# Performance work log

Measured on AMD Instinct MI355X. Metric: run time of the kernel, lower is better.

## Reference

```python
import jax, jax.numpy as jnp
import numpy as np

N = 50000
E = 800000
IN_DIM = 128
HID = 128
OUT = 40


def setup_inputs() -> dict:
    key = jax.random.key(0)
    k1, k2, k3, k4, k5 = jax.random.split(key, 5)
    x = jax.random.normal(k1, (N, IN_DIM), dtype=jnp.float32)
    edge_index = jax.random.randint(k2, (2, E), 0, N, dtype=jnp.int64)
    # Glorot-ish init for GCNConv weights, zero bias (PyG default bias=True)
    W1 = jax.random.normal(k3, (IN_DIM, HID), dtype=jnp.float32) / np.sqrt(IN_DIM)
    b1 = jnp.zeros((HID,), dtype=jnp.float32)
    W2 = jax.random.normal(k4, (HID, OUT), dtype=jnp.float32) / np.sqrt(HID)
    b2 = jnp.zeros((OUT,), dtype=jnp.float32)
    return {"x": x, "edge_index": edge_index, "W1": W1, "b1": b1, "W2": W2, "b2": b2}


def _gcn_norm(edge_index, n_nodes):
    """Add self-loops and compute symmetric GCN normalization per edge.
    Returns (src, dst, norm) with len E + n_nodes."""
    loops = jnp.arange(n_nodes, dtype=edge_index.dtype)
    src = jnp.concatenate([edge_index[0], loops])
    dst = jnpp_concat = jnp.concatenate([edge_index[1], loops])
    dst = jnp.concatenate([edge_index[1], loops])
    deg = jax.ops.segment_sum(jnp.ones_like(dst, dtype=jnp.float32), dst,
                              num_segments=n_nodes)
    dinv = jnp.where(deg > 0, jax.lax.rsqrt(deg), 0.0)
    norm = dinv[src] * dinv[dst]  # [E + N]
    return src, dst, norm


def _gcn_conv(x, src, dst, norm, W, b, n_nodes):
    xw = x @ W                                  # [N, F_out] transform first
    msg = xw[src] * norm[:, None]               # gather + scale, [E+N, F_out]
    out = jax.ops.segment_sum(msg, dst, num_segments=n_nodes)  # scatter-add
    return out + b


def reference(x, edge_index, W1, b1, W2, b2):
    n = x.shape[0]
    src, dst, norm = _gcn_norm(edge_index, n)
    h = _gcn_conv(x, src, dst, norm, W1, b1, n)
    h = jax.nn.relu(h)
    # dropout is identity in eval mode (training=False)
    h = _gcn_conv(h, src, dst, norm, W2, b2, n)
    return jax.nn.softmax(h, axis=1)
```

## Files before the change

kernel.cpp:

```cpp
#include <hip/hip_runtime.h>
#include <hip/hip_fp16.h>

#define IN_DIM 128
#define HID    128
#define OUTC   40
#define CAP    64
#define LSTR   136

typedef _Float16 f16x8 __attribute__((ext_vector_type(8)));
typedef _Float16 f16x4 __attribute__((ext_vector_type(4)));
typedef float    f32x4 __attribute__((ext_vector_type(4)));

__global__ __launch_bounds__(256) void k_scatter(const int* __restrict__ edge, int* __restrict__ cnt,
                                                 int* __restrict__ col,
                                                 const float* __restrict__ W1, const float* __restrict__ W2,
                                                 _Float16* __restrict__ W1T, _Float16* __restrict__ W2T,
                                                 int E, int n, int nbE) {
  int b = blockIdx.x;
  if (b < nbE) {
    int e = b * 256 + threadIdx.x;
    if (e >= E) return;
    int sv = edge[e];
    int d  = edge[E + e];
    if ((unsigned)d >= (unsigned)n || (unsigned)sv >= (unsigned)n) return;
    int pos = atomicAdd(&cnt[d], 1);
    if (pos < CAP) col[(size_t)d * CAP + pos] = sv;
  } else {
    int t = (b - nbE) * 256 + threadIdx.x;
    if (t < 128 * 128) {
      int nn = t >> 7, kk = t & 127;
      W1T[t] = (_Float16)W1[kk * 128 + nn];
    }
    if (t < 48 * 128) {
      int nn = t >> 7, kk = t & 127;
      W2T[t] = (nn < OUTC) ? (_Float16)W2[kk * OUTC + nn] : (_Float16)0.f;
    }
  }
}


__global__ __launch_bounds__(256) void k_gemm1(const float* __restrict__ x, const _Float16* __restrict__ W1T,
                                               const int* __restrict__ cnt, __half* __restrict__ out, int n) {
  __shared__ _Float16 sW[128 * LSTR];
  __shared__ _Float16 sX[64 * LSTR];
  int tid = threadIdx.x;
  int i0  = blockIdx.x * 64;

  {
    const uint4* src = (const uint4*)W1T;
    for (int idx = tid; idx < 2048; idx += 256) {
      int nn = idx >> 4, c = idx & 15;
      *(uint4*)&sW[nn * LSTR + c * 8] = src[nn * 16 + c];
    }
  }
  for (int idx = tid; idx < 2048; idx += 256) {
    int r = idx >> 5, c = idx & 31;
    int row = i0 + r;
    float4 v = (row < n) ? *(const float4*)&x[(size_t)row * IN_DIM + c * 4]
                         : make_float4(0.f, 0.f, 0.f, 0.f);
    f16x4 hv; hv[0] = (_Float16)v.x; hv[1] = (_Float16)v.y; hv[2] = (_Float16)v.z; hv[3] = (_Float16)v.w;
    *(f16x4*)&sX[r * LSTR + c * 4] = hv;
  }
  __syncthreads();

  int wv = tid >> 6, lane = tid & 63;
  int m = lane & 15, quad = lane >> 4;

  const _Float16* ax = &sX[(16 * wv + m) * LSTR + quad * 8];
  f16x8 a0 = *(const f16x8*)(ax);
  f16x8 a1 = *(const f16x8*)(ax + 32);
  f16x8 a2 = *(const f16x8*)(ax + 64);
  f16x8 a3 = *(const f16x8*)(ax + 96);

  int base_row = i0 + 16 * wv + quad * 4;
  float dvr[4];
#pragma unroll
  for (int r = 0; r < 4; ++r) {
    int row = base_row + r;
    dvr[r] = (row < n) ? rsqrtf((float)(cnt[row] + 1)) : 0.f;
  }

#pragma unroll
  for (int t = 0; t < 8; ++t) {
    const _Float16* bx = &sW[(t * 16 + m) * LSTR + quad * 8];
    f16x8 b0 = *(const f16x8*)(bx);
    f16x8 b1 = *(const f16x8*)(bx + 32);
    f16x8 b2 = *(const f16x8*)(bx + 64);
    f16x8 b3 = *(const f16x8*)(bx + 96);
    f32x4 c = {0.f, 0.f, 0.f, 0.f};
    c = __builtin_amdgcn_mfma_f32_16x16x32_f16(a0, b0, c, 0, 0, 0);
    c = __builtin_amdgcn_mfma_f32_16x16x32_f16(a1, b1, c, 0, 0, 0);
    c = __builtin_amdgcn_mfma_f32_16x16x32_f16(a2, b2, c, 0, 0, 0);
    c = __builtin_amdgcn_mfma_f32_16x16x32_f16(a3, b3, c, 0, 0, 0);
    int colb = t * 16 + m;
#pragma unroll
    for (int r = 0; r < 4; ++r) {
      int row = base_row + r;
      if (row < n) out[(size_t)row * HID + colb] = __float2half(c[r] * dvr[r]);
    }
  }
}


__global__ __launch_bounds__(256) void k_agg1(const __half2* __restrict__ xws, const int* __restrict__ cnt,
                                              const int* __restrict__ col, const float* __restrict__ b1,
                                              __half2* __restrict__ h, int n) {
  int wid  = (blockIdx.x * 256 + threadIdx.x) >> 6;
  int lane = threadIdx.x & 63;
  if (wid >= n) return;
  float2 acc = __half22float2(xws[(size_t)wid * 64 + lane]);
  int deg = cnt[wid];
  int end = min(deg, CAP);
  const int* cp = &col[(size_t)wid * CAP];
  int e = 0;
  for (; e + 8 <= end; e += 8) {
    int s0 = cp[e], s1 = cp[e+1], s2 = cp[e+2], s3 = cp[e+3];
    int s4 = cp[e+4], s5 = cp[e+5], s6 = cp[e+6], s7 = cp[e+7];
    float2 v0 = __half22float2(xws[(size_t)s0 * 64 + lane]);
    float2 v1 = __half22float2(xws[(size_t)s1 * 64 + lane]);
    float2 v2 = __half22float2(xws[(size_t)s2 * 64 + lane]);
    float2 v3 = __half22float2(xws[(size_t)s3 * 64 + lane]);
    float2 v4 = __half22float2(xws[(size_t)s4 * 64 + lane]);
    float2 v5 = __half22float2(xws[(size_t)s5 * 64 + lane]);
    float2 v6 = __half22float2(xws[(size_t)s6 * 64 + lane]);
    float2 v7 = __half22float2(xws[(size_t)s7 * 64 + lane]);
    acc.x += (v0.x + v1.x) + (v2.x + v3.x) + ((v4.x + v5.x) + (v6.x + v7.x));
    acc.y += (v0.y + v1.y) + (v2.y + v3.y) + ((v4.y + v5.y) + (v6.y + v7.y));
  }
  for (; e < end; ++e) {
    float2 v = __half22float2(xws[(size_t)cp[e] * 64 + lane]);
    acc.x += v.x; acc.y += v.y;
  }
  float dv = rsqrtf((float)(deg + 1));
  float2 bb = ((const float2*)b1)[lane];
  h[(size_t)wid * 64 + lane] =
      __floats2half2_rn(fmaxf(acc.x * dv + bb.x, 0.f), fmaxf(acc.y * dv + bb.y, 0.f));
}


__global__ __launch_bounds__(256) void k_gemm2(const __half* __restrict__ h, const _Float16* __restrict__ W2T,
                                               const int* __restrict__ cnt, __half* __restrict__ out, int n) {
  __shared__ _Float16 sW[48 * LSTR];
  __shared__ _Float16 sH[64 * LSTR];
  int tid = threadIdx.x;
  int i0  = blockIdx.x * 64;

  {
    const uint4* src = (const uint4*)W2T;
    for (int idx = tid; idx < 768; idx += 256) {
      int nn = idx >> 4, c = idx & 15;
      *(uint4*)&sW[nn * LSTR + c * 8] = src[nn * 16 + c];
    }
  }
  {
    const uint4* src = (const uint4*)h;
    for (int idx = tid; idx < 1024; idx += 256) {
      int r = idx >> 4, c = idx & 15;
      int row = i0 + r;
      uint4 v = (row < n) ? src[(size_t)row * 16 + c] : make_uint4(0u, 0u, 0u, 0u);
      *(uint4*)&sH[r * LSTR + c * 8] = v;
    }
  }
  __syncthreads();

  int wv = tid >> 6, lane = tid & 63;
  int m = lane & 15, quad = lane >> 4;

  const _Float16* ax = &sH[(16 * wv + m) * LSTR + quad * 8];
  f16x8 a0 = *(const f16x8*)(ax);
  f16x8 a1 = *(const f16x8*)(ax + 32);
  f16x8 a2 = *(const f16x8*)(ax + 64);
  f16x8 a3 = *(const f16x8*)(ax + 96);

  int base_row = i0 + 16 * wv + quad * 4;
  float dvr[4];
#pragma unroll
  for (int r = 0; r < 4; ++r) {
    int row = base_row + r;
    dvr[r] = (row < n) ? rsqrtf((float)(cnt[row] + 1)) : 0.f;
  }

#pragma unroll
  for (int t = 0; t < 3; ++t) {
    const _Float16* bx = &sW[(t * 16 + m) * LSTR + quad * 8];
    f16x8 b0 = *(const f16x8*)(bx);
    f16x8 b1 = *(const f16x8*)(bx + 32);
    f16x8 b2 = *(const f16x8*)(bx + 64);
    f16x8 b3 = *(const f16x8*)(bx + 96);
    f32x4 c = {0.f, 0.f, 0.f, 0.f};
    c = __builtin_amdgcn_mfma_f32_16x16x32_f16(a0, b0, c, 0, 0, 0);
    c = __builtin_amdgcn_mfma_f32_16x16x32_f16(a1, b1, c, 0, 0, 0);
    c = __builtin_amdgcn_mfma_f32_16x16x32_f16(a2, b2, c, 0, 0, 0);
    c = __builtin_amdgcn_mfma_f32_16x16x32_f16(a3, b3, c, 0, 0, 0);
    int colb = t * 16 + m;
    if (colb < OUTC) {
#pragma unroll
      for (int r = 0; r < 4; ++r) {
        int row = base_row + r;
        if (row < n) out[(size_t)row * OUTC + colb] = __float2half(c[r] * dvr[r]);
      }
    }
  }
}


__global__ __launch_bounds__(256) void k_agg2(const __half* __restrict__ hw, const int* __restrict__ cnt,
                                              const int* __restrict__ col, const float* __restrict__ b2,
                                              float* __restrict__ out, int n) {
  int wid  = (blockIdx.x * 256 + threadIdx.x) >> 6;
  int lane = threadIdx.x & 63;
  if (wid >= n) return;
  bool act = lane < OUTC;
  int li = act ? lane : 0;
  float acc = act ? __half2float(hw[(size_t)wid * OUTC + li]) : 0.f;
  int deg = cnt[wid];
  int end = min(deg, CAP);
  const int* cp = &col[(size_t)wid * CAP];
  int e = 0;
  for (; e + 8 <= end; e += 8) {
    int s0 = cp[e], s1 = cp[e+1], s2 = cp[e+2], s3 = cp[e+3];
    int s4 = cp[e+4], s5 = cp[e+5], s6 = cp[e+6], s7 = cp[e+7];
    if (act) {
      float a0 = __half2float(hw[(size_t)s0 * OUTC + li]);
      float a1 = __half2float(hw[(size_t)s1 * OUTC + li]);
      float a2 = __half2float(hw[(size_t)s2 * OUTC + li]);
      float a3 = __half2float(hw[(size_t)s3 * OUTC + li]);
      float a4 = __half2float(hw[(size_t)s4 * OUTC + li]);
      float a5 = __half2float(hw[(size_t)s5 * OUTC + li]);
      float a6 = __half2float(hw[(size_t)s6 * OUTC + li]);
      float a7 = __half2float(hw[(size_t)s7 * OUTC + li]);
      acc += (a0 + a1) + (a2 + a3) + ((a4 + a5) + (a6 + a7));
    }
  }
  for (; e < end; ++e) {
    int s = cp[e];
    if (act) acc += __half2float(hw[(size_t)s * OUTC + li]);
  }
  float logit = acc * rsqrtf((float)(deg + 1)) + (act ? b2[lane] : 0.f);
  float m = act ? logit : -1e30f;
#pragma unroll
  for (int o = 32; o > 0; o >>= 1) m = fmaxf(m, __shfl_xor(m, o, 64));
  float ex = act ? __expf(logit - m) : 0.f;
  float sum = ex;
#pragma unroll
  for (int o = 32; o > 0; o >>= 1) sum += __shfl_xor(sum, o, 64);
  if (act) out[(size_t)wid * OUTC + lane] = ex / sum;
}


extern "C" void kernel_launch(void* const* d_in, const int* in_sizes, int n_in,
                              void* d_out, int out_size, void* d_ws, size_t ws_size,
                              hipStream_t stream) {
  const float* x    = (const float*)d_in[0];
  const int*   edge = (const int*)d_in[1];
  const float* W1   = (const float*)d_in[2];
  const float* b1   = (const float*)d_in[3];
  const float* W2   = (const float*)d_in[4];
  const float* b2   = (const float*)d_in[5];
  float* out = (float*)d_out;

  int N = in_sizes[0] / IN_DIM;
  int E = in_sizes[1] / 2;

  char* ws = (char*)d_ws;
  size_t off = 0;
  auto carve = [&](size_t bytes) { char* p = ws + off; off = (off + bytes + 255) & ~(size_t)255; return p; };
  int*      cnt = (int*)carve((size_t)N * 4);
  int*      col = (int*)carve((size_t)N * CAP * 4);
  _Float16* W1T = (_Float16*)carve((size_t)128 * 128 * 2);
  _Float16* W2T = (_Float16*)carve((size_t)48 * 128 * 2);
  __half*   xws = (__half*)carve((size_t)N * HID * 2);
  __half*   h   = (__half*)carve((size_t)N * HID * 2);
  __half*   hw  = xws;

  hipMemsetAsync(cnt, 0, (size_t)N * 4, stream);

  int nbE = (E + 255) / 256;
  k_scatter<<<nbE + 64, 256, 0, stream>>>(edge, cnt, col, W1, W2, W1T, W2T, E, N, nbE);

  k_gemm1<<<(N + 63) / 64, 256, 0, stream>>>(x, W1T, cnt, xws, N);
  k_agg1<<<(N * 64 + 255) / 256, 256, 0, stream>>>((const __half2*)xws, cnt, col, b1, (__half2*)h, N);
  k_gemm2<<<(N + 63) / 64, 256, 0, stream>>>(h, W2T, cnt, hw, N);
  k_agg2<<<(N * 64 + 255) / 256, 256, 0, stream>>>(hw, cnt, col, b2, out, N);
}
```

Before: 226.8 us.

## Partition edge scatter by destination across XCD-aligned block groups

The edge scatter becomes a grid-stride loop in which each group of blocks (blockIdx mod 8) handles only destinations whose low three bits match the group. cnt and col are stored in a permuted node order so each group writes a contiguous region. The aim is to keep atomics and column-list writes local to one XCD's L2 and avoid cross-die cache-line contention. In exchange, every group rescans the full destination array, and every consumer kernel needs a permuted index lookup.

Measured after the change: 220.1 us. -3.0%, faster.

```diff
diff --git a/kernel.cpp b/kernel.cpp
--- a/kernel.cpp
+++ b/kernel.cpp
@@ -11,22 +11,16 @@
 typedef _Float16 f16x4 __attribute__((ext_vector_type(4)));
 typedef float    f32x4 __attribute__((ext_vector_type(4)));
 
+__device__ __forceinline__ int permi(int d, int NP8) { return (d & 7) * NP8 + (d >> 3); }
+
 __global__ __launch_bounds__(256) void k_scatter(const int* __restrict__ edge, int* __restrict__ cnt,
                                                  int* __restrict__ col,
                                                  const float* __restrict__ W1, const float* __restrict__ W2,
                                                  _Float16* __restrict__ W1T, _Float16* __restrict__ W2T,
-                                                 int E, int n, int nbE) {
+                                                 int E, int n, int nbS, int NP8) {
   int b = blockIdx.x;
-  if (b < nbE) {
-    int e = b * 256 + threadIdx.x;
-    if (e >= E) return;
-    int sv = edge[e];
-    int d  = edge[E + e];
-    if ((unsigned)d >= (unsigned)n || (unsigned)sv >= (unsigned)n) return;
-    int pos = atomicAdd(&cnt[d], 1);
-    if (pos < CAP) col[(size_t)d * CAP + pos] = sv;
-  } else {
-    int t = (b - nbE) * 256 + threadIdx.x;
+  if (b >= nbS) {
+    int t = (b - nbS) * 256 + threadIdx.x;
     if (t < 128 * 128) {
       int nn = t >> 7, kk = t & 127;
       W1T[t] = (_Float16)W1[kk * 128 + nn];
@@ -35,12 +29,26 @@
       int nn = t >> 7, kk = t & 127;
       W2T[t] = (nn < OUTC) ? (_Float16)W2[kk * OUTC + nn] : (_Float16)0.f;
     }
+    return;
+  }
+  int g       = b & 7;
+  int tid     = (b >> 3) * 256 + threadIdx.x;
+  int gstride = (nbS >> 3) * 256;
+  for (int e = tid; e < E; e += gstride) {
+    int d = edge[E + e];
+    if ((unsigned)d >= (unsigned)n || (d & 7) != g) continue;
+    int sv = edge[e];
+    if ((unsigned)sv >= (unsigned)n) continue;
+    int p   = g * NP8 + (d >> 3);
+    int pos = atomicAdd(&cnt[p], 1);
+    if (pos < CAP) col[(size_t)p * CAP + pos] = sv;
   }
 }
 
 
 __global__ __launch_bounds__(256) void k_gemm1(const float* __restrict__ x, const _Float16* __restrict__ W1T,
-                                               const int* __restrict__ cnt, __half* __restrict__ out, int n) {
+                                               const int* __restrict__ cnt, __half* __restrict__ out,
+                                               int n, int NP8) {
   __shared__ _Float16 sW[128 * LSTR];
   __shared__ _Float16 sX[64 * LSTR];
   int tid = threadIdx.x;
@@ -77,7 +85,7 @@
 #pragma unroll
   for (int r = 0; r < 4; ++r) {
     int row = base_row + r;
-    dvr[r] = (row < n) ? rsqrtf((float)(cnt[row] + 1)) : 0.f;
+    dvr[r] = (row < n) ? rsqrtf((float)(cnt[permi(row, NP8)] + 1)) : 0.f;
   }
 
 #pragma unroll
@@ -104,14 +112,15 @@
 
 __global__ __launch_bounds__(256) void k_agg1(const __half2* __restrict__ xws, const int* __restrict__ cnt,
                                               const int* __restrict__ col, const float* __restrict__ b1,
-                                              __half2* __restrict__ h, int n) {
+                                              __half2* __restrict__ h, int n, int NP8) {
   int wid  = (blockIdx.x * 256 + threadIdx.x) >> 6;
   int lane = threadIdx.x & 63;
   if (wid >= n) return;
   float2 acc = __half22float2(xws[(size_t)wid * 64 + lane]);
-  int deg = cnt[wid];
+  int p   = permi(wid, NP8);
+  int deg = cnt[p];
   int end = min(deg, CAP);
-  const int* cp = &col[(size_t)wid * CAP];
+  const int* cp = &col[(size_t)p * CAP];
   int e = 0;
   for (; e + 8 <= end; e += 8) {
     int s0 = cp[e], s1 = cp[e+1], s2 = cp[e+2], s3 = cp[e+3];
@@ -139,7 +148,8 @@
 
 
 __global__ __launch_bounds__(256) void k_gemm2(const __half* __restrict__ h, const _Float16* __restrict__ W2T,
-                                               const int* __restrict__ cnt, __half* __restrict__ out, int n) {
+                                               const int* __restrict__ cnt, __half* __restrict__ out,
+                                               int n, int NP8) {
   __shared__ _Float16 sW[48 * LSTR];
   __shared__ _Float16 sH[64 * LSTR];
   int tid = threadIdx.x;
@@ -177,7 +187,7 @@
 #pragma unroll
   for (int r = 0; r < 4; ++r) {
     int row = base_row + r;
-    dvr[r] = (row < n) ? rsqrtf((float)(cnt[row] + 1)) : 0.f;
+    dvr[r] = (row < n) ? rsqrtf((float)(cnt[permi(row, NP8)] + 1)) : 0.f;
   }
 
 #pragma unroll
@@ -206,16 +216,17 @@
 
 __global__ __launch_bounds__(256) void k_agg2(const __half* __restrict__ hw, const int* __restrict__ cnt,
                                               const int* __restrict__ col, const float* __restrict__ b2,
-                                              float* __restrict__ out, int n) {
+                                              float* __restrict__ out, int n, int NP8) {
   int wid  = (blockIdx.x * 256 + threadIdx.x) >> 6;
   int lane = threadIdx.x & 63;
   if (wid >= n) return;
   bool act = lane < OUTC;
   int li = act ? lane : 0;
   float acc = act ? __half2float(hw[(size_t)wid * OUTC + li]) : 0.f;
-  int deg = cnt[wid];
+  int p   = permi(wid, NP8);
+  int deg = cnt[p];
   int end = min(deg, CAP);
-  const int* cp = &col[(size_t)wid * CAP];
+  const int* cp = &col[(size_t)p * CAP];
   int e = 0;
   for (; e + 8 <= end; e += 8) {
     int s0 = cp[e], s1 = cp[e+1], s2 = cp[e+2], s3 = cp[e+3];
@@ -259,27 +270,29 @@
   const float* b2   = (const float*)d_in[5];
   float* out = (float*)d_out;
 
-  int N = in_sizes[0] / IN_DIM;
-  int E = in_sizes[1] / 2;
+  int N   = in_sizes[0] / IN_DIM;
+  int E   = in_sizes[1] / 2;
+  int NP8 = (N + 7) / 8;
+  int NP  = NP8 * 8;
 
   char* ws = (char*)d_ws;
   size_t off = 0;
   auto carve = [&](size_t bytes) { char* p = ws + off; off = (off + bytes + 255) & ~(size_t)255; return p; };
-  int*      cnt = (int*)carve((size_t)N * 4);
-  int*      col = (int*)carve((size_t)N * CAP * 4);
+  int*      cnt = (int*)carve((size_t)NP * 4);
+  int*      col = (int*)carve((size_t)NP * CAP * 4);
   _Float16* W1T = (_Float16*)carve((size_t)128 * 128 * 2);
   _Float16* W2T = (_Float16*)carve((size_t)48 * 128 * 2);
   __half*   xws = (__half*)carve((size_t)N * HID * 2);
   __half*   h   = (__half*)carve((size_t)N * HID * 2);
   __half*   hw  = xws;
 
-  hipMemsetAsync(cnt, 0, (size_t)N * 4, stream);
-
-  int nbE = (E + 255) / 256;
-  k_scatter<<<nbE + 64, 256, 0, stream>>>(edge, cnt, col, W1, W2, W1T, W2T, E, N, nbE);
-
-  k_gemm1<<<(N + 63) / 64, 256, 0, stream>>>(x, W1T, cnt, xws, N);
-  k_agg1<<<(N * 64 + 255) / 256, 256, 0, stream>>>((const __half2*)xws, cnt, col, b1, (__half2*)h, N);
-  k_gemm2<<<(N + 63) / 64, 256, 0, stream>>>(h, W2T, cnt, hw, N);
-  k_agg2<<<(N * 64 + 255) / 256, 256, 0, stream>>>(hw, cnt, col, b2, out, N);
-}
+  hipMemsetAsync(cnt, 0, (size_t)NP * 4, stream);
+
+  int nbS = 1024;
+  k_scatter<<<nbS + 64, 256, 0, stream>>>(edge, cnt, col, W1, W2, W1T, W2T, E, N, nbS, NP8);
+
+  k_gemm1<<<(N + 63) / 64, 256, 0, stream>>>(x, W1T, cnt, xws, N, NP8);
+  k_agg1<<<(N * 64 + 255) / 256, 256, 0, stream>>>((const __half2*)xws, cnt, col, b1, (__half2*)h, N, NP8);
+  k_gemm2<<<(N + 63) / 64, 256, 0, stream>>>(h, W2T, cnt, hw, N, NP8);
+  k_agg2<<<(N * 64 + 255) / 256, 256, 0, stream>>>(hw, cnt, col, b2, out, N, NP8);
+}
```
